# Kernel optimization log

Hardware: AMD Instinct MI355X
Metric: run time of the kernel (lower is better)

Reference implementation:

```python
import jax, jax.numpy as jnp
import numpy as np

HEADS = 8
DIM = 512


def setup_inputs() -> dict:
    key = jax.random.key(0)
    ks = jax.random.split(key, 7)
    B, N, L, C = 2, 64, 32, DIM
    feat1 = jax.random.normal(ks[0], (B, N, L, C), dtype=jnp.float32)
    feat2 = jax.random.normal(ks[1], (B, N, L, C), dtype=jnp.float32)
    s = 1.0 / np.sqrt(C)
    Wq1 = jax.random.normal(ks[2], (C, C), dtype=jnp.float32) * s
    Wk1 = jax.random.normal(ks[3], (C, C), dtype=jnp.float32) * s
    Wq2 = jax.random.normal(ks[4], (C, C), dtype=jnp.float32) * s
    Wk2 = jax.random.normal(ks[5], (C, C), dtype=jnp.float32) * s
    tau = jnp.array(0.3, dtype=jnp.float32)
    return {"feat1": feat1, "feat2": feat2, "Wq1": Wq1, "Wk1": Wk1,
            "Wq2": Wq2, "Wk2": Wk2, "tau": tau}


def _proj_heads(x_flat, W, B, NL, H):
    # nn.Linear(bias=False): y = x @ W.T ; then split heads -> (B, H, NL, hd)
    y = jnp.einsum('btc,dc->btd', x_flat, W)
    return y.reshape(B, NL, H, -1).transpose(0, 2, 1, 3)


def _pooled_scores(Q, Kt, scale, tau, B, H, N, L):
    # scores (B,H,NL,NL) -> softmax -> view (B,H,N,L,N,L) -> amax(-1) -> mean(L) -> mean(H)
    s = jnp.einsum('bhqd,bhkd->bhqk', Q, Kt) * (scale / tau)
    s = jax.nn.softmax(s, axis=-1)
    s = s.reshape(B, H, N, L, N, L)
    s = s.max(axis=-1)          # (B,H,N,L,N)
    s = s.mean(axis=3)          # (B,H,N,N)
    return s.mean(axis=1)       # (B,N,N)


def reference(feat1, feat2, Wq1, Wk1, Wq2, Wk2, tau):
    B, N, L, C = feat1.shape
    H = HEADS
    NL = N * L
    scale = C ** (-0.5)
    f1 = feat1.reshape(B, NL, C)
    f2 = feat2.reshape(B, NL, C)
    Q1 = _proj_heads(f1, Wq1, B, NL, H)
    K1 = _proj_heads(f1, Wk1, B, NL, H)
    Q2 = _proj_heads(f2, Wq2, B, NL, H)
    K2 = _proj_heads(f2, Wk2, B, NL, H)
    c12 = _pooled_scores(Q1, K2, scale, tau, B, H, N, L)
    c21 = _pooled_scores(Q2, K1, scale, tau, B, H, N, L)
    return (c12 + c21) * 0.5
```

## Files before the change

kernel.cpp:

```cpp
#include <hip/hip_runtime.h>
#include <hip/hip_bf16.h>

#define NLQ 2048
#define CDIM 512
#define HD 64
#define NHEADS 8

typedef __attribute__((ext_vector_type(8))) short bf16x8;
typedef __attribute__((ext_vector_type(4))) float f32x4;

#define MFMA(A, B, Cc) __builtin_amdgcn_mfma_f32_16x16x32_bf16(A, B, Cc, 0, 0, 0)

__device__ __forceinline__ short f2bf(float x) {
    __hip_bfloat16 h = __float2bfloat16(x);
    return *reinterpret_cast<short*>(&h);
}

__device__ __forceinline__ float fast_exp2(float x) {
    float r;
    asm("v_exp_f32 %0, %1" : "=v"(r) : "v"(x));
    return r;
}

__device__ __forceinline__ int swz(int row, int colByte) {
    return ((row << 7) + colByte) ^ ((row & 7) << 4);
}

#define QK_ELEMS   8388608
#define X_ELEMS    2097152
#define W_ELEMS    262144
#define PLANE      2097152

__global__ __launch_bounds__(256) void convert_kernel(
    const float* __restrict__ f1, const float* __restrict__ f2,
    const float* __restrict__ Wq1, const float* __restrict__ Wk1,
    const float* __restrict__ Wq2, const float* __restrict__ Wk2,
    const float* __restrict__ tau, short* __restrict__ ws)
{
    short* Xb1 = ws + QK_ELEMS;
    short* Xb2 = Xb1 + X_ELEMS;
    short* Wb  = Xb2 + X_ELEMS;
    float la = 0.044194173824159216f * 1.4426950408889634f / tau[0];

    int bid = blockIdx.x;
    const float* src; short* dst; float a = 1.0f; int idx;
    if (bid < 1024)       { src = f1; dst = Xb1; idx = bid; }
    else if (bid < 2048)  { src = f2; dst = Xb2; idx = bid - 1024; }
    else {
        int wseg = (bid - 2048) >> 7;
        idx = (bid - 2048) & 127;
        src = (wseg == 0) ? Wq1 : (wseg == 1) ? Wk1 : (wseg == 2) ? Wq2 : Wk2;
        dst = Wb + wseg * W_ELEMS;
        a = (wseg == 0 || wseg == 2) ? la : 1.0f;
    }
    int off = idx * 2048 + threadIdx.x * 8;
    float4 x0 = *(const float4*)(src + off);
    float4 x1 = *(const float4*)(src + off + 4);
    bf16x8 v = { f2bf(x0.x * a), f2bf(x0.y * a), f2bf(x0.z * a), f2bf(x0.w * a),
                 f2bf(x1.x * a), f2bf(x1.y * a), f2bf(x1.z * a), f2bf(x1.w * a) };
    *(bf16x8*)(dst + off) = v;
}

__global__ __launch_bounds__(256) void proj_kernel(short* __restrict__ ws)
{
    int bid = blockIdx.x;
    int gx = bid >> 8;
    int mt = (bid >> 3) & 31;
    int nt = bid & 7;

    const short* X   = ws + QK_ELEMS + gx * X_ELEMS;
    const short* Wst = ws + QK_ELEMS + 2 * X_ELEMS + gx * (2 * W_ELEMS);
    short* Yb = ws;

    __shared__ alignas(16) short Alds[2][8192];
    __shared__ alignas(16) short Blds[2][8192];

    int t = threadIdx.x;
    int lane = t & 63;
    int w = t >> 6;
    int wr = w >> 1, wc = w & 1;
    int m0 = mt * 128, d0 = nt * 128;

    int srow = t >> 1;
    int sh = (t & 1) * 32;
    const short* xsrc = X   + (m0 + srow) * CDIM + sh;
    const short* wsrc = Wst + (d0 + srow) * CDIM + sh;

    f32x4 acc[4][4] = {};

    bf16x8 wv0 = *(const bf16x8*)(wsrc);
    bf16x8 wv1 = *(const bf16x8*)(wsrc + 8);
    bf16x8 wv2 = *(const bf16x8*)(wsrc + 16);
    bf16x8 wv3 = *(const bf16x8*)(wsrc + 24);
    bf16x8 xv0 = *(const bf16x8*)(xsrc);
    bf16x8 xv1 = *(const bf16x8*)(xsrc + 8);
    bf16x8 xv2 = *(const bf16x8*)(xsrc + 16);
    bf16x8 xv3 = *(const bf16x8*)(xsrc + 24);
    {
        int b0 = sh * 2;
        *(bf16x8*)((char*)Alds[0] + swz(srow, b0))      = wv0;
        *(bf16x8*)((char*)Alds[0] + swz(srow, b0 + 16)) = wv1;
        *(bf16x8*)((char*)Alds[0] + swz(srow, b0 + 32)) = wv2;
        *(bf16x8*)((char*)Alds[0] + swz(srow, b0 + 48)) = wv3;
        *(bf16x8*)((char*)Blds[0] + swz(srow, b0))      = xv0;
        *(bf16x8*)((char*)Blds[0] + swz(srow, b0 + 16)) = xv1;
        *(bf16x8*)((char*)Blds[0] + swz(srow, b0 + 32)) = xv2;
        *(bf16x8*)((char*)Blds[0] + swz(srow, b0 + 48)) = xv3;
    }
    __syncthreads();

    for (int kc = 0; kc < 8; ++kc) {
        int cur = kc & 1;
        if (kc < 7) {
            const short* xn = xsrc + (kc + 1) * 64;
            const short* wn = wsrc + (kc + 1) * 64;
            wv0 = *(const bf16x8*)(wn);      wv1 = *(const bf16x8*)(wn + 8);
            wv2 = *(const bf16x8*)(wn + 16); wv3 = *(const bf16x8*)(wn + 24);
            xv0 = *(const bf16x8*)(xn);      xv1 = *(const bf16x8*)(xn + 8);
            xv2 = *(const bf16x8*)(xn + 16); xv3 = *(const bf16x8*)(xn + 24);
        }
        int cb = (lane >> 4) << 4;
        bf16x8 bfr[4][2];
        #pragma unroll
        for (int ms = 0; ms < 4; ++ms) {
            int row = (wr << 6) + (ms << 4) + (lane & 15);
            bfr[ms][0] = *(const bf16x8*)((const char*)Blds[cur] + swz(row, cb));
            bfr[ms][1] = *(const bf16x8*)((const char*)Blds[cur] + swz(row, cb + 64));
        }
        #pragma unroll
        for (int ns = 0; ns < 4; ++ns) {
            int arow = (wc << 6) + (ns << 4) + (lane & 15);
            bf16x8 a0 = *(const bf16x8*)((const char*)Alds[cur] + swz(arow, cb));
            bf16x8 a1 = *(const bf16x8*)((const char*)Alds[cur] + swz(arow, cb + 64));
            #pragma unroll
            for (int ms = 0; ms < 4; ++ms) {
                acc[ms][ns] = MFMA(a0, bfr[ms][0], acc[ms][ns]);
                acc[ms][ns] = MFMA(a1, bfr[ms][1], acc[ms][ns]);
            }
        }
        if (kc < 7) {
            int nx = cur ^ 1;
            int b0 = sh * 2;
            *(bf16x8*)((char*)Alds[nx] + swz(srow, b0))      = wv0;
            *(bf16x8*)((char*)Alds[nx] + swz(srow, b0 + 16)) = wv1;
            *(bf16x8*)((char*)Alds[nx] + swz(srow, b0 + 32)) = wv2;
            *(bf16x8*)((char*)Alds[nx] + swz(srow, b0 + 48)) = wv3;
            *(bf16x8*)((char*)Blds[nx] + swz(srow, b0))      = xv0;
            *(bf16x8*)((char*)Blds[nx] + swz(srow, b0 + 16)) = xv1;
            *(bf16x8*)((char*)Blds[nx] + swz(srow, b0 + 32)) = xv2;
            *(bf16x8*)((char*)Blds[nx] + swz(srow, b0 + 48)) = xv3;
        }
        __syncthreads();
    }

    #pragma unroll
    for (int ms = 0; ms < 4; ++ms) {
        int m = m0 + (wr << 6) + (ms << 4) + (lane & 15);
        int bb = m >> 11, tl = m & 2047;
        #pragma unroll
        for (int ns = 0; ns < 4; ++ns) {
            int d = d0 + (wc << 6) + (ns << 4) + ((lane >> 4) << 2);
            int plane = (gx << 1) + (d >> 9);
            int head = (d >> 6) & 7;
            int hd = d & 63;
            short4 v = { f2bf(acc[ms][ns][0]), f2bf(acc[ms][ns][1]),
                         f2bf(acc[ms][ns][2]), f2bf(acc[ms][ns][3]) };
            *(short4*)(Yb + plane * PLANE + ((bb * NHEADS + head) * NLQ + tl) * HD + hd) = v;
        }
    }
}


#define LOADK(buf, ii) do { \
    const short* _k = kp + (ii) * 4096; \
    buf[0][0] = *(const bf16x8*)(_k);        buf[0][1] = *(const bf16x8*)(_k + 32);   \
    buf[1][0] = *(const bf16x8*)(_k + 1024); buf[1][1] = *(const bf16x8*)(_k + 1056); \
    buf[2][0] = *(const bf16x8*)(_k + 2048); buf[2][1] = *(const bf16x8*)(_k + 2080); \
    buf[3][0] = *(const bf16x8*)(_k + 3072); buf[3][1] = *(const bf16x8*)(_k + 3104); \
} while (0)

#define COMPUTE(buf, ii) do { \
    int _kt = (w << 3) + (ii); \
    _Pragma("unroll") \
    for (int qs = 0; qs < 4; ++qs) { \
        f32x4 c0 = {}, c1 = {}, c2 = {}, c3 = {}; \
        c0 = MFMA(buf[0][0], qb[qs][0], c0); c0 = MFMA(buf[0][1], qb[qs][1], c0); \
        c1 = MFMA(buf[1][0], qb[qs][0], c1); c1 = MFMA(buf[1][1], qb[qs][1], c1); \
        c2 = MFMA(buf[2][0], qb[qs][0], c2); c2 = MFMA(buf[2][1], qb[qs][1], c2); \
        c3 = MFMA(buf[3][0], qb[qs][0], c3); c3 = MFMA(buf[3][1], qb[qs][1], c3); \
        float g0 = (fast_exp2(c0[0]) + fast_exp2(c0[1])) + (fast_exp2(c0[2]) + fast_exp2(c0[3])); \
        float g1 = (fast_exp2(c1[0]) + fast_exp2(c1[1])) + (fast_exp2(c1[2]) + fast_exp2(c1[3])); \
        float g2 = (fast_exp2(c2[0]) + fast_exp2(c2[1])) + (fast_exp2(c2[2]) + fast_exp2(c2[3])); \
        float g3 = (fast_exp2(c3[0]) + fast_exp2(c3[1])) + (fast_exp2(c3[2]) + fast_exp2(c3[3])); \
        ps[qs] += (g0 + g1) + (g2 + g3); \
        float a0 = fmaxf(fmaxf(c0[0], c0[1]), c0[2]); \
        float a1 = fmaxf(fmaxf(c0[3], c1[0]), c1[1]); \
        float bm0 = fmaxf(fmaxf(a0, a1), fmaxf(c1[2], c1[3])); \
        float a2 = fmaxf(fmaxf(c2[0], c2[1]), c2[2]); \
        float a3 = fmaxf(fmaxf(c2[3], c3[0]), c3[1]); \
        float bm1 = fmaxf(fmaxf(a2, a3), fmaxf(c3[2], c3[3])); \
        bm0 = fmaxf(bm0, __shfl_xor(bm0, 16)); \
        bm0 = fmaxf(bm0, __shfl_xor(bm0, 32)); \
        bm1 = fmaxf(bm1, __shfl_xor(bm1, 16)); \
        bm1 = fmaxf(bm1, __shfl_xor(bm1, 32)); \
        if (lane < 16) { \
            bms[2 * _kt][(qs << 4) + lane]     = bm0; \
            bms[2 * _kt + 1][(qs << 4) + lane] = bm1; \
        } \
    } \
} while (0)

__global__ __launch_bounds__(256) void attn_kernel(
    const short* __restrict__ qk, float* __restrict__ out)
{
    int bid = blockIdx.x;
    int combo = bid & 31;
    int qt = bid >> 5;
    int h    = combo & 7;
    int pair = (combo >> 3) & 1;
    int b    = combo >> 4;

    const short* Q = qk + (pair ? 2 : 0) * PLANE + (b * NHEADS + h) * NLQ * HD;
    const short* K = qk + (pair ? 1 : 3) * PLANE + (b * NHEADS + h) * NLQ * HD;

    __shared__ float bms[64][65];
    __shared__ float psums[4][64];
    __shared__ float rowinv[64];
    __shared__ float partial[4][64];

    int t = threadIdx.x;
    int lane = t & 63;
    int w = t >> 6;

    bf16x8 qb[4][2];
    #pragma unroll
    for (int qs = 0; qs < 4; ++qs) {
        int row = qt * 64 + (qs << 4) + (lane & 15);
        const short* qp = Q + row * HD + ((lane >> 4) << 3);
        qb[qs][0] = *(const bf16x8*)qp;
        qb[qs][1] = *(const bf16x8*)(qp + 32);
    }

    const short* kp = K + ((w << 9) + (lane & 15)) * HD + ((lane >> 4) << 3);

    float ps[4] = {0.f, 0.f, 0.f, 0.f};

    bf16x8 afA[4][2], afB[4][2];
    LOADK(afA, 0);

    #pragma unroll 1
    for (int i = 0; i < 8; i += 2) {
        LOADK(afB, i + 1);
        COMPUTE(afA, i);
        if (i < 6) LOADK(afA, i + 2);
        COMPUTE(afB, i + 1);
    }

    #pragma unroll
    for (int qs = 0; qs < 4; ++qs) {
        float s = ps[qs];
        s += __shfl_xor(s, 16);
        s += __shfl_xor(s, 32);
        if (lane < 16) psums[w][(qs << 4) + lane] = s;
    }
    __syncthreads();
    if (t < 64) rowinv[t] = 1.0f /
        ((psums[0][t] + psums[1][t]) + (psums[2][t] + psums[3][t]));
    __syncthreads();

    {
        int n2 = t & 63;
        int rg = t >> 6;
        float a = 0.f;
        #pragma unroll
        for (int r = rg * 16; r < rg * 16 + 16; ++r)
            a += fast_exp2(bms[n2][r]) * rowinv[r];
        partial[rg][n2] = a;
    }
    __syncthreads();

    if (t < 128) {
        int n1l = t >> 6, n2 = t & 63;
        float val = (partial[2 * n1l][n2] + partial[2 * n1l + 1][n2]) * (1.0f / 512.0f);
        atomicAdd(&out[(b * 64 + qt * 2 + n1l) * 64 + n2], val);
    }
}

extern "C" void kernel_launch(void* const* d_in, const int* in_sizes, int n_in,
                              void* d_out, int out_size, void* d_ws, size_t ws_size,
                              hipStream_t stream) {
    const float* f1  = (const float*)d_in[0];
    const float* f2  = (const float*)d_in[1];
    const float* Wq1 = (const float*)d_in[2];
    const float* Wk1 = (const float*)d_in[3];
    const float* Wq2 = (const float*)d_in[4];
    const float* Wk2 = (const float*)d_in[5];
    const float* tau = (const float*)d_in[6];
    float* out = (float*)d_out;
    short* ws = (short*)d_ws;

    hipMemsetAsync(d_out, 0, (size_t)out_size * sizeof(float), stream);
    convert_kernel<<<dim3(2560), dim3(256), 0, stream>>>(f1, f2, Wq1, Wk1, Wq2, Wk2, tau, ws);
    proj_kernel<<<dim3(512), dim3(256), 0, stream>>>(ws);
    attn_kernel<<<dim3(1024), dim3(256), 0, stream>>>(ws, out);
}
```

Before: 135.7 us.

## Use 512-thread blocks in projection GEMM and raise MFMA priority in attention

The projection kernel now runs 8 waves per 128x128 tile instead of 4. Each wave computes a 64x32 sub-tile, and each thread stages half as much global data per k-step, which cuts per-thread register pressure and adds more waves to hide latency. The attention kernel wraps its MFMA sequence in s_setprio raise/lower so matrix instructions get issue priority over other waves. The cost is that each wave reloads the B fragments it shares with the other waves, so LDS read traffic per MFMA rises.

```diff
diff --git a/kernel.cpp b/kernel.cpp
--- a/kernel.cpp
+++ b/kernel.cpp
@@ -61,7 +61,7 @@
     *(bf16x8*)(dst + off) = v;
 }
 
-__global__ __launch_bounds__(256) void proj_kernel(short* __restrict__ ws)
+__global__ __launch_bounds__(512) void proj_kernel(short* __restrict__ ws)
 {
     int bid = blockIdx.x;
     int gx = bid >> 8;
@@ -78,34 +78,27 @@
     int t = threadIdx.x;
     int lane = t & 63;
     int w = t >> 6;
-    int wr = w >> 1, wc = w & 1;
+    int wr = w >> 2;
+    int wc = w & 3;
     int m0 = mt * 128, d0 = nt * 128;
 
-    int srow = t >> 1;
-    int sh = (t & 1) * 32;
-    const short* xsrc = X   + (m0 + srow) * CDIM + sh;
-    const short* wsrc = Wst + (d0 + srow) * CDIM + sh;
-
-    f32x4 acc[4][4] = {};
-
-    bf16x8 wv0 = *(const bf16x8*)(wsrc);
-    bf16x8 wv1 = *(const bf16x8*)(wsrc + 8);
-    bf16x8 wv2 = *(const bf16x8*)(wsrc + 16);
-    bf16x8 wv3 = *(const bf16x8*)(wsrc + 24);
-    bf16x8 xv0 = *(const bf16x8*)(xsrc);
-    bf16x8 xv1 = *(const bf16x8*)(xsrc + 8);
-    bf16x8 xv2 = *(const bf16x8*)(xsrc + 16);
-    bf16x8 xv3 = *(const bf16x8*)(xsrc + 24);
+    int srow = t >> 2;
+    int sc   = (t & 3) * 16;
+    const short* xsrc = X   + (m0 + srow) * CDIM + sc;
+    const short* wsrc = Wst + (d0 + srow) * CDIM + sc;
+
+    f32x4 acc[4][2] = {};
+
+    bf16x8 xa = *(const bf16x8*)(xsrc);
+    bf16x8 xb = *(const bf16x8*)(xsrc + 8);
+    bf16x8 wa = *(const bf16x8*)(wsrc);
+    bf16x8 wb = *(const bf16x8*)(wsrc + 8);
     {
-        int b0 = sh * 2;
-        *(bf16x8*)((char*)Alds[0] + swz(srow, b0))      = wv0;
-        *(bf16x8*)((char*)Alds[0] + swz(srow, b0 + 16)) = wv1;
-        *(bf16x8*)((char*)Alds[0] + swz(srow, b0 + 32)) = wv2;
-        *(bf16x8*)((char*)Alds[0] + swz(srow, b0 + 48)) = wv3;
-        *(bf16x8*)((char*)Blds[0] + swz(srow, b0))      = xv0;
-        *(bf16x8*)((char*)Blds[0] + swz(srow, b0 + 16)) = xv1;
-        *(bf16x8*)((char*)Blds[0] + swz(srow, b0 + 32)) = xv2;
-        *(bf16x8*)((char*)Blds[0] + swz(srow, b0 + 48)) = xv3;
+        int b0 = sc * 2;
+        *(bf16x8*)((char*)Alds[0] + swz(srow, b0))      = wa;
+        *(bf16x8*)((char*)Alds[0] + swz(srow, b0 + 16)) = wb;
+        *(bf16x8*)((char*)Blds[0] + swz(srow, b0))      = xa;
+        *(bf16x8*)((char*)Blds[0] + swz(srow, b0 + 16)) = xb;
     }
     __syncthreads();
 
@@ -114,10 +107,8 @@
         if (kc < 7) {
             const short* xn = xsrc + (kc + 1) * 64;
             const short* wn = wsrc + (kc + 1) * 64;
-            wv0 = *(const bf16x8*)(wn);      wv1 = *(const bf16x8*)(wn + 8);
-            wv2 = *(const bf16x8*)(wn + 16); wv3 = *(const bf16x8*)(wn + 24);
-            xv0 = *(const bf16x8*)(xn);      xv1 = *(const bf16x8*)(xn + 8);
-            xv2 = *(const bf16x8*)(xn + 16); xv3 = *(const bf16x8*)(xn + 24);
+            xa = *(const bf16x8*)(xn); xb = *(const bf16x8*)(xn + 8);
+            wa = *(const bf16x8*)(wn); wb = *(const bf16x8*)(wn + 8);
         }
         int cb = (lane >> 4) << 4;
         bf16x8 bfr[4][2];
@@ -128,8 +119,8 @@
             bfr[ms][1] = *(const bf16x8*)((const char*)Blds[cur] + swz(row, cb + 64));
         }
         #pragma unroll
-        for (int ns = 0; ns < 4; ++ns) {
-            int arow = (wc << 6) + (ns << 4) + (lane & 15);
+        for (int ns = 0; ns < 2; ++ns) {
+            int arow = (wc << 5) + (ns << 4) + (lane & 15);
             bf16x8 a0 = *(const bf16x8*)((const char*)Alds[cur] + swz(arow, cb));
             bf16x8 a1 = *(const bf16x8*)((const char*)Alds[cur] + swz(arow, cb + 64));
             #pragma unroll
@@ -140,15 +131,11 @@
         }
         if (kc < 7) {
             int nx = cur ^ 1;
-            int b0 = sh * 2;
-            *(bf16x8*)((char*)Alds[nx] + swz(srow, b0))      = wv0;
-            *(bf16x8*)((char*)Alds[nx] + swz(srow, b0 + 16)) = wv1;
-            *(bf16x8*)((char*)Alds[nx] + swz(srow, b0 + 32)) = wv2;
-            *(bf16x8*)((char*)Alds[nx] + swz(srow, b0 + 48)) = wv3;
-            *(bf16x8*)((char*)Blds[nx] + swz(srow, b0))      = xv0;
-            *(bf16x8*)((char*)Blds[nx] + swz(srow, b0 + 16)) = xv1;
-            *(bf16x8*)((char*)Blds[nx] + swz(srow, b0 + 32)) = xv2;
-            *(bf16x8*)((char*)Blds[nx] + swz(srow, b0 + 48)) = xv3;
+            int b0 = sc * 2;
+            *(bf16x8*)((char*)Alds[nx] + swz(srow, b0))      = wa;
+            *(bf16x8*)((char*)Alds[nx] + swz(srow, b0 + 16)) = wb;
+            *(bf16x8*)((char*)Blds[nx] + swz(srow, b0))      = xa;
+            *(bf16x8*)((char*)Blds[nx] + swz(srow, b0 + 16)) = xb;
         }
         __syncthreads();
     }
@@ -158,8 +145,8 @@
         int m = m0 + (wr << 6) + (ms << 4) + (lane & 15);
         int bb = m >> 11, tl = m & 2047;
         #pragma unroll
-        for (int ns = 0; ns < 4; ++ns) {
-            int d = d0 + (wc << 6) + (ns << 4) + ((lane >> 4) << 2);
+        for (int ns = 0; ns < 2; ++ns) {
+            int d = d0 + (wc << 5) + (ns << 4) + ((lane >> 4) << 2);
             int plane = (gx << 1) + (d >> 9);
             int head = (d >> 6) & 7;
             int hd = d & 63;
@@ -169,7 +156,6 @@
         }
     }
 }
-
 
 #define LOADK(buf, ii) do { \
     const short* _k = kp + (ii) * 4096; \
@@ -184,10 +170,12 @@
     _Pragma("unroll") \
     for (int qs = 0; qs < 4; ++qs) { \
         f32x4 c0 = {}, c1 = {}, c2 = {}, c3 = {}; \
+        __builtin_amdgcn_s_setprio(1); \
         c0 = MFMA(buf[0][0], qb[qs][0], c0); c0 = MFMA(buf[0][1], qb[qs][1], c0); \
         c1 = MFMA(buf[1][0], qb[qs][0], c1); c1 = MFMA(buf[1][1], qb[qs][1], c1); \
         c2 = MFMA(buf[2][0], qb[qs][0], c2); c2 = MFMA(buf[2][1], qb[qs][1], c2); \
         c3 = MFMA(buf[3][0], qb[qs][0], c3); c3 = MFMA(buf[3][1], qb[qs][1], c3); \
+        __builtin_amdgcn_s_setprio(0); \
         float g0 = (fast_exp2(c0[0]) + fast_exp2(c0[1])) + (fast_exp2(c0[2]) + fast_exp2(c0[3])); \
         float g1 = (fast_exp2(c1[0]) + fast_exp2(c1[1])) + (fast_exp2(c1[2]) + fast_exp2(c1[3])); \
         float g2 = (fast_exp2(c2[0]) + fast_exp2(c2[1])) + (fast_exp2(c2[2]) + fast_exp2(c2[3])); \
@@ -301,6 +289,6 @@
 
     hipMemsetAsync(d_out, 0, (size_t)out_size * sizeof(float), stream);
     convert_kernel<<<dim3(2560), dim3(256), 0, stream>>>(f1, f2, Wq1, Wk1, Wq2, Wk2, tau, ws);
-    proj_kernel<<<dim3(512), dim3(256), 0, stream>>>(ws);
+    proj_kernel<<<dim3(512), dim3(512), 0, stream>>>(ws);
     attn_kernel<<<dim3(1024), dim3(256), 0, stream>>>(ws, out);
 }
```

New measurement: 136.3 us. No clear change (+0.4%).
